# Kernel optimization log

Hardware: AMD Instinct MI355X
Metric: run time of the kernel (lower is better)

The kernel has to match this reference:

```python
import jax, jax.numpy as jnp
import numpy as np

B, LQ, LK, DQ, DK, DV, H = 8, 256, 1024, 512, 512, 512, 128
NEG = -1000000.0

def setup_inputs() -> dict:
    key = jax.random.key(0)
    kq, kk, kv, kl, kwq, kwk, kwv = jax.random.split(key, 7)
    return {
        "Q": jax.random.normal(kq, (B, LQ, DQ), dtype=jnp.float32),
        "K": jax.random.normal(kk, (B, LK, DK), dtype=jnp.float32),
        "V": jax.random.normal(kv, (B, LK, DV), dtype=jnp.float32),
        "valid_lengths": jax.random.randint(kl, (B,), 1, LK + 1),
        "W_q": jax.random.normal(kwq, (DQ, H), dtype=jnp.float32) / np.sqrt(DQ),
        "W_k": jax.random.normal(kwk, (DK, H), dtype=jnp.float32) / np.sqrt(DK),
        "w_v": jax.random.normal(kwv, (H,), dtype=jnp.float32) / np.sqrt(H),
    }

def reference(Q, K, V, valid_lengths, W_q, W_k, w_v):
    # Projections
    q = Q @ W_q                      # (B, LQ, H)
    k = K @ W_k                      # (B, LK, H)
    # Additive (Bahdanau) features: broadcast add + tanh
    feat = jnp.tanh(q[:, :, None, :] + k[:, None, :, :])  # (B, LQ, LK, H)
    scores = jnp.einsum('bqkh,h->bqk', feat, w_v)          # (B, LQ, LK)
    # Masked softmax over keys (valid_lengths broadcast over all queries)
    mask = jnp.arange(LK)[None, None, :] < valid_lengths[:, None, None]
    scores = jnp.where(mask, scores, NEG)
    attn = jax.nn.softmax(scores, axis=-1)                 # (B, LQ, LK)
    # dropout_rate = 0.0 -> identity
    return jnp.einsum('bqk,bkd->bqd', attn, V)             # (B, LQ, DV)
```

## Files before the change

### kernel.cpp

```cpp
#include <hip/hip_runtime.h>

#define NBATCH 8
#define NLQ    256
#define NLK    1024
#define NDQ    512
#define NDV    512
#define NH     128
#define NEGV   -1000000.0f
#define TANH_SCALE 2.8853900817779268f
#define LOG2E      1.4426950408889634f

using f16x8 = __attribute__((ext_vector_type(8))) _Float16;
using f16x4 = __attribute__((ext_vector_type(4))) _Float16;
using f32x4 = __attribute__((ext_vector_type(4))) float;

__device__ __forceinline__ float fast_exp2(float x) {
#if __has_builtin(__builtin_amdgcn_exp2f)
  return __builtin_amdgcn_exp2f(x);
#else
  return exp2f(x);
#endif
}
__device__ __forceinline__ float fast_rcp(float x) {
#if __has_builtin(__builtin_amdgcn_rcpf)
  return __builtin_amdgcn_rcpf(x);
#else
  return 1.0f / x;
#endif
}

__global__ __launch_bounds__(256)
void prep_wT_kernel(const float* __restrict__ Wq, const float* __restrict__ Wk,
                    _Float16* __restrict__ wT) {
  const int idx = blockIdx.x * 256 + threadIdx.x;
  const int n = idx & 127;
  const int k = (idx >> 7) & 511;
  const int s = idx >> 16;
  const float* W = s ? Wk : Wq;
  wT[((size_t)(s * NH + n)) * NDQ + k] = (_Float16)W[k * NH + n];
}

__global__ __launch_bounds__(256)
void proj_mfma_kernel(const float* __restrict__ Q, const float* __restrict__ Kin,
                      const _Float16* __restrict__ wT,
                      float* __restrict__ qp, float* __restrict__ ekT) {
  const int bx = blockIdx.x;
  const int nq = blockIdx.y;
  const bool isQ = (bx < 32);
  const float* A = isQ ? Q : Kin;
  const int m0 = (isQ ? bx : bx - 32) * 64;
  const int sIdx = isQ ? 0 : 1;

  const int w = threadIdx.x >> 6, lane = threadIdx.x & 63;
  const int mrow = m0 + w * 16 + (lane & 15);
  const int kseg = (lane >> 4) * 8;

  const float* aBase = A + (size_t)mrow * NDQ + kseg;
  const _Float16* wt0 = wT + ((size_t)(sIdx * NH + nq * 32 +      (lane & 15))) * NDQ + kseg;
  const _Float16* wt1 = wT + ((size_t)(sIdx * NH + nq * 32 + 16 + (lane & 15))) * NDQ + kseg;

  f32x4 acc0 = {}, acc1 = {};
#pragma unroll 4
  for (int k0 = 0; k0 < NDQ; k0 += 32) {
    const float4 a0 = *(const float4*)&aBase[k0];
    const float4 a1 = *(const float4*)&aBase[k0 + 4];
    f16x8 af;
    af[0] = (_Float16)a0.x; af[1] = (_Float16)a0.y;
    af[2] = (_Float16)a0.z; af[3] = (_Float16)a0.w;
    af[4] = (_Float16)a1.x; af[5] = (_Float16)a1.y;
    af[6] = (_Float16)a1.z; af[7] = (_Float16)a1.w;
    const f16x8 b0 = *(const f16x8*)&wt0[k0];
    const f16x8 b1 = *(const f16x8*)&wt1[k0];
    acc0 = __builtin_amdgcn_mfma_f32_16x16x32_f16(af, b0, acc0, 0, 0, 0);
    acc1 = __builtin_amdgcn_mfma_f32_16x16x32_f16(af, b1, acc1, 0, 0, 0);
  }

  const int orow = m0 + w * 16 + (lane >> 4) * 4;
  const int col0 = nq * 32 + (lane & 15);
  if (isQ) {
#pragma unroll
    for (int r = 0; r < 4; ++r) {
      qp[(size_t)(orow + r) * NH + col0]      = fast_exp2(acc0[r] * TANH_SCALE);
      qp[(size_t)(orow + r) * NH + col0 + 16] = fast_exp2(acc1[r] * TANH_SCALE);
    }
  } else {
#pragma unroll
    for (int r = 0; r < 4; ++r) {
      const int grow = orow + r;
      const int b = grow >> 10, key = grow & 1023;
      ekT[((size_t)(b * NH) + col0)      * NLK + key] = fast_exp2(acc0[r] * TANH_SCALE);
      ekT[((size_t)(b * NH) + col0 + 16) * NLK + key] = fast_exp2(acc1[r] * TANH_SCALE);
    }
  }
}

__global__ __launch_bounds__(256)
void scores_kernel(const float* __restrict__ qp, const float* __restrict__ ekT,
                   const float* __restrict__ wv, float* __restrict__ sc) {
  const int w = threadIdx.x >> 6;
  const int lane = threadIdx.x & 63;
  const int seg = blockIdx.x * 4 + w;
  const int qg  = blockIdx.y;
  const int b   = blockIdx.z;
  const int key0 = seg * 128 + lane * 2;

  const float* kcol  = &ekT[(size_t)b * NH * NLK + key0];
  const float* qbase = &qp[(size_t)(b * NLQ + qg * 4) * NH];

  float2 acc[4] = {};
#pragma unroll 8
  for (int g = 0; g < 32; ++g) {
    const float4 w4 = *(const float4*)&wv[g * 4];
    float4 q4[4];
#pragma unroll
    for (int qi = 0; qi < 4; ++qi)
      q4[qi] = *(const float4*)&qbase[qi * NH + g * 4];
#pragma unroll
    for (int hh = 0; hh < 4; ++hh) {
      const float2 kv = *(const float2*)&kcol[(size_t)(g * 4 + hh) * NLK];
      const float wl = (hh == 0) ? w4.x : (hh == 1) ? w4.y : (hh == 2) ? w4.z : w4.w;
#pragma unroll
      for (int qi = 0; qi < 4; ++qi) {
        const float qs = (hh == 0) ? q4[qi].x : (hh == 1) ? q4[qi].y
                       : (hh == 2) ? q4[qi].z : q4[qi].w;
        acc[qi].x = fmaf(wl, fast_rcp(fmaf(qs, kv.x, 1.0f)), acc[qi].x);
        acc[qi].y = fmaf(wl, fast_rcp(fmaf(qs, kv.y, 1.0f)), acc[qi].y);
      }
    }
  }

#pragma unroll
  for (int qi = 0; qi < 4; ++qi) {
    float2 o;
    o.x = -2.0f * acc[qi].x;
    o.y = -2.0f * acc[qi].y;
    *(float2*)&sc[(size_t)(b * NLQ + qg * 4 + qi) * NLK + key0] = o;
  }
}

__global__ __launch_bounds__(256)
void softmax_kernel(float* __restrict__ sc, const int* __restrict__ vlen) {
  const int row = blockIdx.x * 4 + (threadIdx.x >> 6);
  const int lane = threadIdx.x & 63;
  const int VL = vlen[row >> 8];
  float* base = &sc[(size_t)row * NLK];

  float s[16];
#pragma unroll
  for (int g = 0; g < 4; ++g) {
    const int k0 = (g * 64 + lane) * 4;
    const float4 v = *(const float4*)&base[k0];
    s[g * 4 + 0] = (k0 + 0 < VL) ? v.x : NEGV;
    s[g * 4 + 1] = (k0 + 1 < VL) ? v.y : NEGV;
    s[g * 4 + 2] = (k0 + 2 < VL) ? v.z : NEGV;
    s[g * 4 + 3] = (k0 + 3 < VL) ? v.w : NEGV;
  }

  float m = s[0];
#pragma unroll
  for (int t = 1; t < 16; ++t) m = fmaxf(m, s[t]);
#pragma unroll
  for (int off = 32; off > 0; off >>= 1) m = fmaxf(m, __shfl_xor(m, off));

  float p[16];
  float sum = 0.0f;
#pragma unroll
  for (int t = 0; t < 16; ++t) {
    p[t] = fast_exp2((s[t] - m) * LOG2E);
    sum += p[t];
  }
#pragma unroll
  for (int off = 32; off > 0; off >>= 1) sum += __shfl_xor(sum, off);
  const float inv = fast_rcp(sum);

  _Float16* hbase = (_Float16*)base;
#pragma unroll
  for (int g = 0; g < 4; ++g) {
    const int k0 = (g * 64 + lane) * 4;
    f16x4 h;
    h[0] = (_Float16)(p[g * 4 + 0] * inv);
    h[1] = (_Float16)(p[g * 4 + 1] * inv);
    h[2] = (_Float16)(p[g * 4 + 2] * inv);
    h[3] = (_Float16)(p[g * 4 + 3] * inv);
    *(f16x4*)&hbase[k0] = h;
  }
}

__global__ __launch_bounds__(256)
void pv_mfma_kernel(const _Float16* __restrict__ attnH, const float* __restrict__ V,
                    float* __restrict__ out) {
  const int b  = blockIdx.z;
  const int m0 = blockIdx.x * 64;
  const int n0 = blockIdx.y * 64;
  const int tid = threadIdx.x;
  const int w = tid >> 6, lane = tid & 63;

  __shared__ _Float16 aT[64][40];
  __shared__ _Float16 vT[64][32];

  const _Float16* aBase = attnH + (size_t)(b * NLQ + m0) * 2048;
  const float*    vBase = V + (size_t)b * NLK * NDV + n0;
  float*          oBase = out + (size_t)(b * NLQ + m0) * NDV + n0;

  const int ar = tid >> 2;
  const int ak = (tid & 3) * 8;
  const int vk = tid >> 4;
  const int vn = (tid & 15) * 4;
  const int vswz = ((vn >> 2) & 3) << 3;

  const int am  = w * 16 + (lane & 15);
  const int akf = (lane >> 4) * 8;
  const int bn  = lane & 15;
  const int bks = akf ^ (((bn >> 2) & 3) << 3);

  f32x4 acc0 = {}, acc1 = {}, acc2 = {}, acc3 = {};

  float4 aReg = *(const float4*)&aBase[(size_t)ar * 2048 + ak];
  float4 vReg0 = *(const float4*)&vBase[(size_t)(vk) * NDV + vn];
  float4 vReg1 = *(const float4*)&vBase[(size_t)(16 + vk) * NDV + vn];

  for (int k0 = 0; k0 < NLK; k0 += 32) {
    __syncthreads();
    *(float4*)&aT[ar][ak] = aReg;
    {
      const int ks0 = vk ^ vswz;
      vT[vn + 0][ks0] = (_Float16)vReg0.x;
      vT[vn + 1][ks0] = (_Float16)vReg0.y;
      vT[vn + 2][ks0] = (_Float16)vReg0.z;
      vT[vn + 3][ks0] = (_Float16)vReg0.w;
      const int ks1 = (16 + vk) ^ vswz;
      vT[vn + 0][ks1] = (_Float16)vReg1.x;
      vT[vn + 1][ks1] = (_Float16)vReg1.y;
      vT[vn + 2][ks1] = (_Float16)vReg1.z;
      vT[vn + 3][ks1] = (_Float16)vReg1.w;
    }
    __syncthreads();

    if (k0 + 32 < NLK) {
      aReg = *(const float4*)&aBase[(size_t)ar * 2048 + k0 + 32 + ak];
      vReg0 = *(const float4*)&vBase[(size_t)(k0 + 32 + vk) * NDV + vn];
      vReg1 = *(const float4*)&vBase[(size_t)(k0 + 48 + vk) * NDV + vn];
    }

    const f16x8 af = *(const f16x8*)&aT[am][akf];
    const f16x8 bf0 = *(const f16x8*)&vT[ 0 + bn][bks];
    const f16x8 bf1 = *(const f16x8*)&vT[16 + bn][bks];
    const f16x8 bf2 = *(const f16x8*)&vT[32 + bn][bks];
    const f16x8 bf3 = *(const f16x8*)&vT[48 + bn][bks];
    acc0 = __builtin_amdgcn_mfma_f32_16x16x32_f16(af, bf0, acc0, 0, 0, 0);
    acc1 = __builtin_amdgcn_mfma_f32_16x16x32_f16(af, bf1, acc1, 0, 0, 0);
    acc2 = __builtin_amdgcn_mfma_f32_16x16x32_f16(af, bf2, acc2, 0, 0, 0);
    acc3 = __builtin_amdgcn_mfma_f32_16x16x32_f16(af, bf3, acc3, 0, 0, 0);
  }

  const int orow = w * 16 + (lane >> 4) * 4;
  const int ocol = lane & 15;
#pragma unroll
  for (int r = 0; r < 4; ++r) {
    oBase[(size_t)(orow + r) * NDV + ocol +  0] = acc0[r];
    oBase[(size_t)(orow + r) * NDV + ocol + 16] = acc1[r];
    oBase[(size_t)(orow + r) * NDV + ocol + 32] = acc2[r];
    oBase[(size_t)(orow + r) * NDV + ocol + 48] = acc3[r];
  }
}

extern "C" void kernel_launch(void* const* d_in, const int* in_sizes, int n_in,
                              void* d_out, int out_size, void* d_ws, size_t ws_size,
                              hipStream_t stream) {
  const float* Q    = (const float*)d_in[0];
  const float* Kin  = (const float*)d_in[1];
  const float* V    = (const float*)d_in[2];
  const int*   vlen = (const int*)d_in[3];
  const float* Wq   = (const float*)d_in[4];
  const float* Wk   = (const float*)d_in[5];
  const float* wv   = (const float*)d_in[6];
  float* out = (float*)d_out;

  float* qp  = (float*)d_ws;
  float* ekT = qp + NBATCH * NLQ * NH;
  float* sc  = ekT + NBATCH * NH * NLK;
  _Float16* wT = (_Float16*)(sc + (size_t)NBATCH * NLQ * NLK);

  hipLaunchKernelGGL(prep_wT_kernel, dim3(2 * NDQ * NH / 256), dim3(256), 0, stream,
                     Wq, Wk, wT);
  hipLaunchKernelGGL(proj_mfma_kernel, dim3(160, 4), dim3(256), 0, stream,
                     Q, Kin, wT, qp, ekT);
  hipLaunchKernelGGL(scores_kernel, dim3(2, 64, NBATCH), dim3(256), 0, stream,
                     qp, ekT, wv, sc);
  hipLaunchKernelGGL(softmax_kernel, dim3(NBATCH * NLQ / 4), dim3(256), 0, stream,
                     sc, vlen);
  hipLaunchKernelGGL(pv_mfma_kernel, dim3(NLQ / 64, NDV / 64, NBATCH), dim3(256), 0, stream,
                     (const _Float16*)sc, V, out);
}
```

Before: 89.30 us.

## Fuse scores and masked softmax into one kernel with block-wide reductions

The scores kernel and the separate softmax kernel become one kernel. Each 512-thread block now covers all 1024 keys for four queries, and the row max and sum are reduced across warps through shared memory. The fp32 score matrix is no longer written to and re-read from global memory; the kernel writes fp16 attention weights straight into a compact buffer. That buffer has an NLK row stride instead of the old 2048-half stride, so the PV kernel reads denser rows. The cost is two block barriers, larger blocks, and half as many blocks for the scores stage, which may lower latency hiding.

Result: faster. 87.42 us (-2.1%).

```diff
diff --git a/kernel.cpp b/kernel.cpp
--- a/kernel.cpp
+++ b/kernel.cpp
@@ -12,6 +12,7 @@
 
 using f16x8 = __attribute__((ext_vector_type(8))) _Float16;
 using f16x4 = __attribute__((ext_vector_type(4))) _Float16;
+using f16x2 = __attribute__((ext_vector_type(2))) _Float16;
 using f32x4 = __attribute__((ext_vector_type(4))) float;
 
 __device__ __forceinline__ float fast_exp2(float x) {
@@ -94,15 +95,18 @@
   }
 }
 
-__global__ __launch_bounds__(256)
-void scores_kernel(const float* __restrict__ qp, const float* __restrict__ ekT,
-                   const float* __restrict__ wv, float* __restrict__ sc) {
+__global__ __launch_bounds__(512)
+void scores_softmax_kernel(const float* __restrict__ qp, const float* __restrict__ ekT,
+                           const float* __restrict__ wv, const int* __restrict__ vlen,
+                           _Float16* __restrict__ attnH) {
+  const int b  = blockIdx.x;
+  const int qg = blockIdx.y;
   const int w = threadIdx.x >> 6;
   const int lane = threadIdx.x & 63;
-  const int seg = blockIdx.x * 4 + w;
-  const int qg  = blockIdx.y;
-  const int b   = blockIdx.z;
-  const int key0 = seg * 128 + lane * 2;
+  const int key0 = w * 128 + lane * 2;
+
+  __shared__ float redm[8][4];
+  __shared__ float reds[8][4];
 
   const float* kcol  = &ekT[(size_t)b * NH * NLK + key0];
   const float* qbase = &qp[(size_t)(b * NLQ + qg * 4) * NH];
@@ -129,60 +133,53 @@
     }
   }
 
-#pragma unroll
-  for (int qi = 0; qi < 4; ++qi) {
-    float2 o;
-    o.x = -2.0f * acc[qi].x;
-    o.y = -2.0f * acc[qi].y;
-    *(float2*)&sc[(size_t)(b * NLQ + qg * 4 + qi) * NLK + key0] = o;
-  }
-}
-
-__global__ __launch_bounds__(256)
-void softmax_kernel(float* __restrict__ sc, const int* __restrict__ vlen) {
-  const int row = blockIdx.x * 4 + (threadIdx.x >> 6);
-  const int lane = threadIdx.x & 63;
-  const int VL = vlen[row >> 8];
-  float* base = &sc[(size_t)row * NLK];
-
-  float s[16];
-#pragma unroll
-  for (int g = 0; g < 4; ++g) {
-    const int k0 = (g * 64 + lane) * 4;
-    const float4 v = *(const float4*)&base[k0];
-    s[g * 4 + 0] = (k0 + 0 < VL) ? v.x : NEGV;
-    s[g * 4 + 1] = (k0 + 1 < VL) ? v.y : NEGV;
-    s[g * 4 + 2] = (k0 + 2 < VL) ? v.z : NEGV;
-    s[g * 4 + 3] = (k0 + 3 < VL) ? v.w : NEGV;
-  }
-
-  float m = s[0];
-#pragma unroll
-  for (int t = 1; t < 16; ++t) m = fmaxf(m, s[t]);
-#pragma unroll
-  for (int off = 32; off > 0; off >>= 1) m = fmaxf(m, __shfl_xor(m, off));
-
-  float p[16];
-  float sum = 0.0f;
-#pragma unroll
-  for (int t = 0; t < 16; ++t) {
-    p[t] = fast_exp2((s[t] - m) * LOG2E);
-    sum += p[t];
-  }
-#pragma unroll
-  for (int off = 32; off > 0; off >>= 1) sum += __shfl_xor(sum, off);
-  const float inv = fast_rcp(sum);
-
-  _Float16* hbase = (_Float16*)base;
-#pragma unroll
-  for (int g = 0; g < 4; ++g) {
-    const int k0 = (g * 64 + lane) * 4;
-    f16x4 h;
-    h[0] = (_Float16)(p[g * 4 + 0] * inv);
-    h[1] = (_Float16)(p[g * 4 + 1] * inv);
-    h[2] = (_Float16)(p[g * 4 + 2] * inv);
-    h[3] = (_Float16)(p[g * 4 + 3] * inv);
-    *(f16x4*)&hbase[k0] = h;
+  const int VL = vlen[b];
+  float2 s[4];
+#pragma unroll
+  for (int qi = 0; qi < 4; ++qi) {
+    s[qi].x = (key0 + 0 < VL) ? -2.0f * acc[qi].x : NEGV;
+    s[qi].y = (key0 + 1 < VL) ? -2.0f * acc[qi].y : NEGV;
+  }
+
+#pragma unroll
+  for (int qi = 0; qi < 4; ++qi) {
+    float m = fmaxf(s[qi].x, s[qi].y);
+#pragma unroll
+    for (int off = 32; off > 0; off >>= 1) m = fmaxf(m, __shfl_xor(m, off));
+    if (lane == 0) redm[w][qi] = m;
+  }
+  __syncthreads();
+  float mg[4];
+#pragma unroll
+  for (int qi = 0; qi < 4; ++qi) {
+    float m = redm[0][qi];
+#pragma unroll
+    for (int ww = 1; ww < 8; ++ww) m = fmaxf(m, redm[ww][qi]);
+    mg[qi] = m;
+  }
+
+  float2 p[4];
+#pragma unroll
+  for (int qi = 0; qi < 4; ++qi) {
+    p[qi].x = fast_exp2((s[qi].x - mg[qi]) * LOG2E);
+    p[qi].y = fast_exp2((s[qi].y - mg[qi]) * LOG2E);
+    float sum = p[qi].x + p[qi].y;
+#pragma unroll
+    for (int off = 32; off > 0; off >>= 1) sum += __shfl_xor(sum, off);
+    if (lane == 0) reds[w][qi] = sum;
+  }
+  __syncthreads();
+
+#pragma unroll
+  for (int qi = 0; qi < 4; ++qi) {
+    float tot = reds[0][qi];
+#pragma unroll
+    for (int ww = 1; ww < 8; ++ww) tot += reds[ww][qi];
+    const float inv = fast_rcp(tot);
+    f16x2 h;
+    h[0] = (_Float16)(p[qi].x * inv);
+    h[1] = (_Float16)(p[qi].y * inv);
+    *(f16x2*)&attnH[(size_t)(b * NLQ + qg * 4 + qi) * NLK + key0] = h;
   }
 }
 
@@ -198,7 +195,7 @@
   __shared__ _Float16 aT[64][40];
   __shared__ _Float16 vT[64][32];
 
-  const _Float16* aBase = attnH + (size_t)(b * NLQ + m0) * 2048;
+  const _Float16* aBase = attnH + (size_t)(b * NLQ + m0) * NLK;
   const float*    vBase = V + (size_t)b * NLK * NDV + n0;
   float*          oBase = out + (size_t)(b * NLQ + m0) * NDV + n0;
 
@@ -215,13 +212,13 @@
 
   f32x4 acc0 = {}, acc1 = {}, acc2 = {}, acc3 = {};
 
-  float4 aReg = *(const float4*)&aBase[(size_t)ar * 2048 + ak];
+  f16x8 aReg = *(const f16x8*)&aBase[(size_t)ar * NLK + ak];
   float4 vReg0 = *(const float4*)&vBase[(size_t)(vk) * NDV + vn];
   float4 vReg1 = *(const float4*)&vBase[(size_t)(16 + vk) * NDV + vn];
 
   for (int k0 = 0; k0 < NLK; k0 += 32) {
     __syncthreads();
-    *(float4*)&aT[ar][ak] = aReg;
+    *(f16x8*)&aT[ar][ak] = aReg;
     {
       const int ks0 = vk ^ vswz;
       vT[vn + 0][ks0] = (_Float16)vReg0.x;
@@ -237,7 +234,7 @@
     __syncthreads();
 
     if (k0 + 32 < NLK) {
-      aReg = *(const float4*)&aBase[(size_t)ar * 2048 + k0 + 32 + ak];
+      aReg = *(const f16x8*)&aBase[(size_t)ar * NLK + k0 + 32 + ak];
       vReg0 = *(const float4*)&vBase[(size_t)(k0 + 32 + vk) * NDV + vn];
       vReg1 = *(const float4*)&vBase[(size_t)(k0 + 48 + vk) * NDV + vn];
     }
@@ -278,17 +275,15 @@
 
   float* qp  = (float*)d_ws;
   float* ekT = qp + NBATCH * NLQ * NH;
-  float* sc  = ekT + NBATCH * NH * NLK;
-  _Float16* wT = (_Float16*)(sc + (size_t)NBATCH * NLQ * NLK);
+  _Float16* attnH = (_Float16*)(ekT + NBATCH * NH * NLK);
+  _Float16* wT = attnH + (size_t)NBATCH * NLQ * NLK;
 
   hipLaunchKernelGGL(prep_wT_kernel, dim3(2 * NDQ * NH / 256), dim3(256), 0, stream,
                      Wq, Wk, wT);
   hipLaunchKernelGGL(proj_mfma_kernel, dim3(160, 4), dim3(256), 0, stream,
                      Q, Kin, wT, qp, ekT);
-  hipLaunchKernelGGL(scores_kernel, dim3(2, 64, NBATCH), dim3(256), 0, stream,
-                     qp, ekT, wv, sc);
-  hipLaunchKernelGGL(softmax_kernel, dim3(NBATCH * NLQ / 4), dim3(256), 0, stream,
-                     sc, vlen);
+  hipLaunchKernelGGL(scores_softmax_kernel, dim3(NBATCH, 64), dim3(512), 0, stream,
+                     qp, ekT, wv, vlen, attnH);
   hipLaunchKernelGGL(pv_mfma_kernel, dim3(NLQ / 64, NDV / 64, NBATCH), dim3(256), 0, stream,
-                     (const _Float16*)sc, V, out);
-}
+                     attnH, V, out);
+}
```

## Skip masked key ranges in projection, scores and PV; halve PV tile width

Applied to the files above, without the earlier changes.

Uses valid_lengths to exit early in the key projection and scores blocks whose key range is fully masked, and bounds the PV loop at the valid length rounded up to 32. The PV kernel tile shrinks from 64 to 32 output columns, doubling the grid so fewer loop iterations per block still fill the GPU. Masked keys still get zero probability from softmax, so skipping them is exact, provided the softmax kernel writes zeros there rather than reading skipped score entries. Blocks finish unevenly across batches because the valid lengths differ.

Measured after the change: 83.19 us. 6.8% less time.

```diff
diff --git a/kernel.cpp b/kernel.cpp
--- a/kernel.cpp
+++ b/kernel.cpp
@@ -12,6 +12,7 @@
 
 using f16x8 = __attribute__((ext_vector_type(8))) _Float16;
 using f16x4 = __attribute__((ext_vector_type(4))) _Float16;
+using f16x2 = __attribute__((ext_vector_type(2))) _Float16;
 using f32x4 = __attribute__((ext_vector_type(4))) float;
 
 __device__ __forceinline__ float fast_exp2(float x) {
@@ -42,7 +43,7 @@
 
 __global__ __launch_bounds__(256)
 void proj_mfma_kernel(const float* __restrict__ Q, const float* __restrict__ Kin,
-                      const _Float16* __restrict__ wT,
+                      const _Float16* __restrict__ wT, const int* __restrict__ vlen,
                       float* __restrict__ qp, float* __restrict__ ekT) {
   const int bx = blockIdx.x;
   const int nq = blockIdx.y;
@@ -50,6 +51,11 @@
   const float* A = isQ ? Q : Kin;
   const int m0 = (isQ ? bx : bx - 32) * 64;
   const int sIdx = isQ ? 0 : 1;
+
+  if (!isQ) {
+    const int b = m0 >> 10;
+    if ((m0 & 1023) >= vlen[b]) return;
+  }
 
   const int w = threadIdx.x >> 6, lane = threadIdx.x & 63;
   const int mrow = m0 + w * 16 + (lane & 15);
@@ -96,13 +102,16 @@
 
 __global__ __launch_bounds__(256)
 void scores_kernel(const float* __restrict__ qp, const float* __restrict__ ekT,
-                   const float* __restrict__ wv, float* __restrict__ sc) {
+                   const float* __restrict__ wv, const int* __restrict__ vlen,
+                   float* __restrict__ sc) {
   const int w = threadIdx.x >> 6;
   const int lane = threadIdx.x & 63;
   const int seg = blockIdx.x * 4 + w;
   const int qg  = blockIdx.y;
   const int b   = blockIdx.z;
   const int key0 = seg * 128 + lane * 2;
+
+  if (seg * 128 >= vlen[b]) return;
 
   const float* kcol  = &ekT[(size_t)b * NH * NLK + key0];
   const float* qbase = &qp[(size_t)(b * NLQ + qg * 4) * NH];
@@ -188,15 +197,16 @@
 
 __global__ __launch_bounds__(256)
 void pv_mfma_kernel(const _Float16* __restrict__ attnH, const float* __restrict__ V,
-                    float* __restrict__ out) {
+                    const int* __restrict__ vlen, float* __restrict__ out) {
   const int b  = blockIdx.z;
   const int m0 = blockIdx.x * 64;
-  const int n0 = blockIdx.y * 64;
+  const int n0 = blockIdx.y * 32;
   const int tid = threadIdx.x;
   const int w = tid >> 6, lane = tid & 63;
+  const int kmax = (vlen[b] + 31) & ~31;
 
   __shared__ _Float16 aT[64][40];
-  __shared__ _Float16 vT[64][32];
+  __shared__ _Float16 vT[32][32];
 
   const _Float16* aBase = attnH + (size_t)(b * NLQ + m0) * 2048;
   const float*    vBase = V + (size_t)b * NLK * NDV + n0;
@@ -204,8 +214,8 @@
 
   const int ar = tid >> 2;
   const int ak = (tid & 3) * 8;
-  const int vk = tid >> 4;
-  const int vn = (tid & 15) * 4;
+  const int vk = tid >> 3;
+  const int vn = (tid & 7) * 4;
   const int vswz = ((vn >> 2) & 3) << 3;
 
   const int am  = w * 16 + (lane & 15);
@@ -213,44 +223,33 @@
   const int bn  = lane & 15;
   const int bks = akf ^ (((bn >> 2) & 3) << 3);
 
-  f32x4 acc0 = {}, acc1 = {}, acc2 = {}, acc3 = {};
-
-  float4 aReg = *(const float4*)&aBase[(size_t)ar * 2048 + ak];
-  float4 vReg0 = *(const float4*)&vBase[(size_t)(vk) * NDV + vn];
-  float4 vReg1 = *(const float4*)&vBase[(size_t)(16 + vk) * NDV + vn];
-
-  for (int k0 = 0; k0 < NLK; k0 += 32) {
+  f32x4 acc0 = {}, acc1 = {};
+
+  f16x8 aReg = *(const f16x8*)&aBase[(size_t)ar * 2048 + ak];
+  float4 vReg = *(const float4*)&vBase[(size_t)vk * NDV + vn];
+
+  for (int k0 = 0; k0 < kmax; k0 += 32) {
     __syncthreads();
-    *(float4*)&aT[ar][ak] = aReg;
+    *(f16x8*)&aT[ar][ak] = aReg;
     {
-      const int ks0 = vk ^ vswz;
-      vT[vn + 0][ks0] = (_Float16)vReg0.x;
-      vT[vn + 1][ks0] = (_Float16)vReg0.y;
-      vT[vn + 2][ks0] = (_Float16)vReg0.z;
-      vT[vn + 3][ks0] = (_Float16)vReg0.w;
-      const int ks1 = (16 + vk) ^ vswz;
-      vT[vn + 0][ks1] = (_Float16)vReg1.x;
-      vT[vn + 1][ks1] = (_Float16)vReg1.y;
-      vT[vn + 2][ks1] = (_Float16)vReg1.z;
-      vT[vn + 3][ks1] = (_Float16)vReg1.w;
+      const int ks = vk ^ vswz;
+      vT[vn + 0][ks] = (_Float16)vReg.x;
+      vT[vn + 1][ks] = (_Float16)vReg.y;
+      vT[vn + 2][ks] = (_Float16)vReg.z;
+      vT[vn + 3][ks] = (_Float16)vReg.w;
     }
     __syncthreads();
 
-    if (k0 + 32 < NLK) {
-      aReg = *(const float4*)&aBase[(size_t)ar * 2048 + k0 + 32 + ak];
-      vReg0 = *(const float4*)&vBase[(size_t)(k0 + 32 + vk) * NDV + vn];
-      vReg1 = *(const float4*)&vBase[(size_t)(k0 + 48 + vk) * NDV + vn];
+    if (k0 + 32 < kmax) {
+      aReg = *(const f16x8*)&aBase[(size_t)ar * 2048 + k0 + 32 + ak];
+      vReg = *(const float4*)&vBase[(size_t)(k0 + 32 + vk) * NDV + vn];
     }
 
     const f16x8 af = *(const f16x8*)&aT[am][akf];
     const f16x8 bf0 = *(const f16x8*)&vT[ 0 + bn][bks];
     const f16x8 bf1 = *(const f16x8*)&vT[16 + bn][bks];
-    const f16x8 bf2 = *(const f16x8*)&vT[32 + bn][bks];
-    const f16x8 bf3 = *(const f16x8*)&vT[48 + bn][bks];
     acc0 = __builtin_amdgcn_mfma_f32_16x16x32_f16(af, bf0, acc0, 0, 0, 0);
     acc1 = __builtin_amdgcn_mfma_f32_16x16x32_f16(af, bf1, acc1, 0, 0, 0);
-    acc2 = __builtin_amdgcn_mfma_f32_16x16x32_f16(af, bf2, acc2, 0, 0, 0);
-    acc3 = __builtin_amdgcn_mfma_f32_16x16x32_f16(af, bf3, acc3, 0, 0, 0);
   }
 
   const int orow = w * 16 + (lane >> 4) * 4;
@@ -259,8 +258,6 @@
   for (int r = 0; r < 4; ++r) {
     oBase[(size_t)(orow + r) * NDV + ocol +  0] = acc0[r];
     oBase[(size_t)(orow + r) * NDV + ocol + 16] = acc1[r];
-    oBase[(size_t)(orow + r) * NDV + ocol + 32] = acc2[r];
-    oBase[(size_t)(orow + r) * NDV + ocol + 48] = acc3[r];
   }
 }
 
@@ -284,11 +281,11 @@
   hipLaunchKernelGGL(prep_wT_kernel, dim3(2 * NDQ * NH / 256), dim3(256), 0, stream,
                      Wq, Wk, wT);
   hipLaunchKernelGGL(proj_mfma_kernel, dim3(160, 4), dim3(256), 0, stream,
-                     Q, Kin, wT, qp, ekT);
+                     Q, Kin, wT, vlen, qp, ekT);
   hipLaunchKernelGGL(scores_kernel, dim3(2, 64, NBATCH), dim3(256), 0, stream,
-                     qp, ekT, wv, sc);
+                     qp, ekT, wv, vlen, sc);
   hipLaunchKernelGGL(softmax_kernel, dim3(NBATCH * NLQ / 4), dim3(256), 0, stream,
                      sc, vlen);
-  hipLaunchKernelGGL(pv_mfma_kernel, dim3(NLQ / 64, NDV / 64, NBATCH), dim3(256), 0, stream,
-                     (const _Float16*)sc, V, out);
-}
+  hipLaunchKernelGGL(pv_mfma_kernel, dim3(NLQ / 64, NDV / 32, NBATCH), dim3(256), 0, stream,
+                     (const _Float16*)sc, V, vlen, out);
+}
```
